# Kernel optimization log

Measured on AMD Instinct MI355X. Metric: run time of the kernel, lower is better.

Reference implementation:

```python
import jax, jax.numpy as jnp
import numpy as np

B, S, D_IN, D_OUT, H = 4, 2048, 1024, 1024, 16
HD = D_OUT // H  # 64


def setup_inputs() -> dict:
    key = jax.random.key(0)
    ks = jax.random.split(key, 6)
    scale_in = 1.0 / np.sqrt(D_IN)
    scale_out = 1.0 / np.sqrt(D_OUT)
    return {
        "x": jax.random.normal(ks[0], (B, S, D_IN), dtype=jnp.float32),
        "Wq": jax.random.normal(ks[1], (D_IN, D_OUT), dtype=jnp.float32) * scale_in,
        "Wk": jax.random.normal(ks[2], (D_IN, D_OUT), dtype=jnp.float32) * scale_in,
        "Wv": jax.random.normal(ks[3], (D_IN, D_OUT), dtype=jnp.float32) * scale_in,
        "Wo": jax.random.normal(ks[4], (D_OUT, D_OUT), dtype=jnp.float32) * scale_out,
        "bo": jax.random.normal(ks[5], (D_OUT,), dtype=jnp.float32) * 0.01,
    }


def reference(x, Wq, Wk, Wv, Wo, bo):
    b, s, _ = x.shape
    # project and split heads: (b, s, d_out) -> (b, h, s, hd)
    def split(t):
        return t.reshape(b, s, H, HD).transpose(0, 2, 1, 3)
    q = split(x @ Wq)
    k = split(x @ Wk)
    v = split(x @ Wv)
    # scaled causal attention scores (b, h, s, s)
    scores = jnp.einsum('bhqd,bhkd->bhqk', q, k) / jnp.sqrt(jnp.float32(HD))
    causal = jnp.tril(jnp.ones((s, s), dtype=bool))
    scores = jnp.where(causal, scores, -jnp.inf)
    weights = jax.nn.softmax(scores, axis=-1)
    # dropout p=0.0 -> identity (eval mode)
    ctx = jnp.einsum('bhqk,bhkd->bhqd', weights, v)
    ctx = ctx.transpose(0, 2, 1, 3).reshape(b, s, D_OUT)
    return ctx @ Wo + bo
```

## Files before the change

### kernel.cpp

```cpp
#include <hip/hip_runtime.h>
#include <stdint.h>

#define DEVINL __device__ __forceinline__

typedef __attribute__((ext_vector_type(8))) __bf16 bf16x8;
typedef __attribute__((ext_vector_type(4))) float f32x4;
typedef __attribute__((ext_vector_type(8))) unsigned short u16x8;
typedef __attribute__((ext_vector_type(2))) unsigned int u32x2;

constexpr int Bc = 4, Sc = 2048, DINc = 1024, Hc = 16;
constexpr float QSCALE = 0.18033688011112042f;

DEVINL unsigned short f2bf(float x) {
  unsigned u = __builtin_bit_cast(unsigned, x);
  u += 0x7fffu + ((u >> 16) & 1u);
  return (unsigned short)(u >> 16);
}

DEVINL unsigned pack_bf16_trunc(float p0, float p1) {
  return __builtin_amdgcn_perm(__builtin_bit_cast(unsigned, p1),
                               __builtin_bit_cast(unsigned, p0), 0x07060302u);
}

DEVINL void gload_lds16(const void* g, void* l) {
  __builtin_amdgcn_global_load_lds(
      (const __attribute__((address_space(1))) void*)g,
      (__attribute__((address_space(3))) void*)l, 16, 0, 0);
}

template <int ROWS>
DEVINL void stage_tile(const unsigned short* g, int ld, void* lds, int tid) {
#pragma unroll
  for (int p = 0; p < ROWS / 32; ++p) {
    int L = (p * 256 + tid) * 16;
    int row = L >> 7;
    int cb = L & 127;
    int scb = cb ^ ((row & 7) << 4);
    gload_lds16((const char*)(g + (size_t)row * ld) + scb, (char*)lds + L);
  }
}

DEVINL bf16x8 read_frag(const void* lds, int row, int kelem) {
  int addr = row * 128 + (((kelem * 2) ^ ((row & 7) << 4)));
  return *(const bf16x8*)((const char*)lds + addr);
}

__global__ __launch_bounds__(256) void prep_inputs(
    const float* __restrict__ x, const float* __restrict__ Wq,
    const float* __restrict__ Wk, const float* __restrict__ Wv,
    const float* __restrict__ Wo, unsigned short* __restrict__ xb,
    unsigned short* __restrict__ wqkvt, unsigned short* __restrict__ wot) {
  __shared__ float t[64][65];
  int bid = blockIdx.x;
  if (bid < 4096) {
    int i = (bid * 256 + threadIdx.x) * 8;
    f32x4 a = *(const f32x4*)(x + i);
    f32x4 b = *(const f32x4*)(x + i + 4);
    u16x8 r;
    r[0] = f2bf(a[0]); r[1] = f2bf(a[1]); r[2] = f2bf(a[2]); r[3] = f2bf(a[3]);
    r[4] = f2bf(b[0]); r[5] = f2bf(b[1]); r[6] = f2bf(b[2]); r[7] = f2bf(b[3]);
    *(u16x8*)(xb + i) = r;
    return;
  }
  int bid2 = bid - 4096;
  int z = bid2 >> 8, rem = bid2 & 255;
  const float* src;
  unsigned short* dst;
  if (z == 0)      { src = Wq; dst = wqkvt; }
  else if (z == 1) { src = Wk; dst = wqkvt + (size_t)1024 * 1024; }
  else if (z == 2) { src = Wv; dst = wqkvt + (size_t)2048 * 1024; }
  else             { src = Wo; dst = wot; }
  int n0 = (rem & 15) * 64, k0 = (rem >> 4) * 64;
  int tx = threadIdx.x & 63, ty = threadIdx.x >> 6;
#pragma unroll
  for (int r = 0; r < 64; r += 4)
    t[r + ty][tx] = src[(size_t)(k0 + r + ty) * 1024 + n0 + tx];
  __syncthreads();
#pragma unroll
  for (int r = 0; r < 64; r += 4)
    dst[(size_t)(n0 + r + ty) * 1024 + k0 + tx] = f2bf(t[tx][r + ty]);
}

__global__ __launch_bounds__(256, 2) void gemm_qkv(
    const unsigned short* __restrict__ A, const unsigned short* __restrict__ Bt,
    unsigned short* __restrict__ qws, unsigned short* __restrict__ kws,
    unsigned short* __restrict__ vtws) {
  __shared__ __align__(16) char lsmem[4 * 128 * 64 * 2];
  unsigned short* lA0 = (unsigned short*)lsmem;
  unsigned short* lB0 = (unsigned short*)(lsmem + 32768);
  int tid = threadIdx.x, lane = tid & 63, wave = tid >> 6;
  int wr = wave >> 1, wc = wave & 1;
  int bm = blockIdx.x, bn = blockIdx.y;
  const unsigned short* Ab = A + (size_t)bm * 128 * 1024;
  const unsigned short* Bb = Bt + (size_t)bn * 128 * 1024;
  int r15 = lane & 15, g4 = lane >> 4, khi = g4 * 8;

  f32x4 acc[4][4];
#pragma unroll
  for (int i = 0; i < 4; ++i)
#pragma unroll
    for (int j = 0; j < 4; ++j) acc[i][j] = (f32x4){0.f, 0.f, 0.f, 0.f};

  int cur = 0;
  stage_tile<128>(Ab, 1024, lA0, tid);
  stage_tile<128>(Bb, 1024, lB0, tid);
#pragma unroll 1
  for (int t = 0; t < 16; ++t) {
    __syncthreads();
    if (t + 1 < 16) {
      stage_tile<128>(Ab + (t + 1) * 64, 1024, lA0 + (cur ^ 1) * 128 * 64, tid);
      stage_tile<128>(Bb + (t + 1) * 64, 1024, lB0 + (cur ^ 1) * 128 * 64, tid);
    }
#pragma unroll
    for (int ks = 0; ks < 2; ++ks) {
      bf16x8 af[4], bfr[4];
#pragma unroll
      for (int i = 0; i < 4; ++i)
        af[i] = read_frag(lA0 + cur * 128 * 64, wr * 64 + i * 16 + r15, ks * 32 + khi);
#pragma unroll
      for (int j = 0; j < 4; ++j)
        bfr[j] = read_frag(lB0 + cur * 128 * 64, wc * 64 + j * 16 + r15, ks * 32 + khi);
      __builtin_amdgcn_s_setprio(1);
#pragma unroll
      for (int i = 0; i < 4; ++i)
#pragma unroll
        for (int j = 0; j < 4; ++j)
          acc[i][j] = __builtin_amdgcn_mfma_f32_16x16x32_bf16(af[i], bfr[j], acc[i][j], 0, 0, 0);
      __builtin_amdgcn_s_setprio(0);
    }
    cur ^= 1;
  }

  int sel = bn >> 3;
  float* sc = (float*)lsmem;
  constexpr int PADW = 132;
  int bq = (bm * 128) >> 11;
#pragma unroll 1
  for (int pass = 0; pass < 2; ++pass) {
    __syncthreads();
    if (wr == pass) {
#pragma unroll
      for (int i = 0; i < 4; ++i)
#pragma unroll
        for (int j = 0; j < 4; ++j)
#pragma unroll
          for (int r = 0; r < 4; ++r) {
            float v = acc[i][j][r];
            if (sel == 0) v *= QSCALE;
            sc[(i * 16 + g4 * 4 + r) * PADW + wc * 64 + j * 16 + r15] = v;
          }
    }
    __syncthreads();
    if (sel < 2) {
      int row = tid >> 2, c0 = (tid & 3) * 32;
      int m = bm * 128 + pass * 64 + row;
      int s = m & 2047;
      int colg = (bn & 7) * 128 + c0;
      int h = colg >> 6, d0 = colg & 63;
      unsigned short* dst =
          (sel == 0 ? qws : kws) + ((size_t)(bq * 16 + h) * 2048 + s) * 64 + d0;
#pragma unroll
      for (int q = 0; q < 4; ++q) {
        f32x4 a = *(const f32x4*)&sc[row * PADW + c0 + q * 8];
        f32x4 b2 = *(const f32x4*)&sc[row * PADW + c0 + q * 8 + 4];
        u16x8 o;
        o[0] = f2bf(a[0]);  o[1] = f2bf(a[1]);  o[2] = f2bf(a[2]);  o[3] = f2bf(a[3]);
        o[4] = f2bf(b2[0]); o[5] = f2bf(b2[1]); o[6] = f2bf(b2[2]); o[7] = f2bf(b2[3]);
        *(u16x8*)(dst + q * 8) = o;
      }
    } else {
      int col = tid >> 1, s0loc = (tid & 1) * 32;
      int colg = (bn & 7) * 128 + col;
      int h = colg >> 6, d = colg & 63;
      int sbase = (bm * 128 + pass * 64 + s0loc) & 2047;
      unsigned short* dst =
          vtws + ((size_t)(bq * 16 + h) * 64 + d) * 2048 + sbase;
#pragma unroll
      for (int q = 0; q < 4; ++q) {
        u16x8 o;
#pragma unroll
        for (int e = 0; e < 8; ++e)
          o[e] = f2bf(sc[(s0loc + q * 8 + e) * PADW + col]);
        *(u16x8*)(dst + q * 8) = o;
      }
    }
  }
}

__global__ __launch_bounds__(256, 3) void attn(
    const unsigned short* __restrict__ qws, const unsigned short* __restrict__ kws,
    const unsigned short* __restrict__ vtws, unsigned short* __restrict__ ctx) {
  __shared__ __align__(16) unsigned short lK[2][64 * 64];
  __shared__ __align__(16) unsigned short lV[2][64 * 64];
  __shared__ __align__(16) unsigned short lP[4][32 * 64];
  int tid = threadIdx.x, lane = tid & 63, wave = tid >> 6;
  int bh = blockIdx.x * 8 + (blockIdx.y & 7);
  int t = 15 - (int)(blockIdx.y >> 3);
  int r15 = lane & 15, g4 = lane >> 4;
  const unsigned short* Kb = kws + (size_t)bh * 2048 * 64;
  const unsigned short* Vb = vtws + (size_t)bh * 64 * 2048;
  int b = bh >> 4, h = bh & 15;
  char* Pw = (char*)&lP[wave][0];

  int q0 = t * 128;
  int myrow0 = q0 + wave * 32;
  const unsigned short* Qb = qws + ((size_t)bh * 2048 + myrow0) * 64;

  bf16x8 qf[2][2];
#pragma unroll
  for (int mf = 0; mf < 2; ++mf)
#pragma unroll
    for (int ks = 0; ks < 2; ++ks)
      qf[mf][ks] = *(const bf16x8*)(Qb + (size_t)(mf * 16 + r15) * 64 + ks * 32 + g4 * 8);

  float m_run[2] = {-1e30f, -1e30f}, l_run[2] = {0.f, 0.f};
  f32x4 o_acc[2][4];
#pragma unroll
  for (int mf = 0; mf < 2; ++mf)
#pragma unroll
    for (int df = 0; df < 4; ++df) o_acc[mf][df] = (f32x4){0.f, 0.f, 0.f, 0.f};

  int nkt = 2 * t + 2;
  int cur = 0;
  stage_tile<64>(Kb, 64, lK[0], tid);
  stage_tile<64>(Vb, 2048, lV[0], tid);

#pragma unroll 1
  for (int kt = 0; kt < nkt; ++kt) {
    __syncthreads();
    if (kt + 1 < nkt) {
      stage_tile<64>(Kb + (size_t)(kt + 1) * 64 * 64, 64, lK[cur ^ 1], tid);
      stage_tile<64>(Vb + (size_t)(kt + 1) * 64, 2048, lV[cur ^ 1], tid);
    }

    f32x4 sacc[2][4];
#pragma unroll
    for (int mf = 0; mf < 2; ++mf)
#pragma unroll
      for (int nf = 0; nf < 4; ++nf) sacc[mf][nf] = (f32x4){0.f, 0.f, 0.f, 0.f};
#pragma unroll
    for (int ks = 0; ks < 2; ++ks) {
      bf16x8 kf[4];
#pragma unroll
      for (int nf = 0; nf < 4; ++nf)
        kf[nf] = read_frag(lK[cur], nf * 16 + r15, ks * 32 + g4 * 8);
      __builtin_amdgcn_s_setprio(1);
#pragma unroll
      for (int mf = 0; mf < 2; ++mf)
#pragma unroll
        for (int nf = 0; nf < 4; ++nf)
          sacc[mf][nf] = __builtin_amdgcn_mfma_f32_16x16x32_bf16(kf[nf], qf[mf][ks], sacc[mf][nf], 0, 0, 0);
      __builtin_amdgcn_s_setprio(0);
    }

    if (kt * 64 + 63 > myrow0) {
#pragma unroll
      for (int mf = 0; mf < 2; ++mf) {
        int q = myrow0 + mf * 16 + r15;
#pragma unroll
        for (int nf = 0; nf < 4; ++nf) {
          int kbase = kt * 64 + nf * 16 + g4 * 4;
#pragma unroll
          for (int r = 0; r < 4; ++r)
            if (kbase + r > q) sacc[mf][nf][r] = -3e38f;
        }
      }
    }

    float tm[2];
#pragma unroll
    for (int mf = 0; mf < 2; ++mf) {
      float a0 = fmaxf(fmaxf(sacc[mf][0][0], sacc[mf][0][1]), fmaxf(sacc[mf][0][2], sacc[mf][0][3]));
      float a1 = fmaxf(fmaxf(sacc[mf][1][0], sacc[mf][1][1]), fmaxf(sacc[mf][1][2], sacc[mf][1][3]));
      float a2 = fmaxf(fmaxf(sacc[mf][2][0], sacc[mf][2][1]), fmaxf(sacc[mf][2][2], sacc[mf][2][3]));
      float a3 = fmaxf(fmaxf(sacc[mf][3][0], sacc[mf][3][1]), fmaxf(sacc[mf][3][2], sacc[mf][3][3]));
      float m = fmaxf(fmaxf(a0, a1), fmaxf(a2, a3));
      m = fmaxf(m, __shfl_xor(m, 16));
      m = fmaxf(m, __shfl_xor(m, 32));
      tm[mf] = m;
    }

    bool ok = (tm[0] <= m_run[0] + 11.5f) & (tm[1] <= m_run[1] + 11.5f);
    if (!__all(ok)) {
#pragma unroll
      for (int mf = 0; mf < 2; ++mf) {
        float mn = fmaxf(m_run[mf], tm[mf]);
        float a = __builtin_amdgcn_exp2f(m_run[mf] - mn);
        m_run[mf] = mn;
        l_run[mf] *= a;
        float av[4];
#pragma unroll
        for (int r = 0; r < 4; ++r)
          av[r] = __shfl(a, (g4 * 4 + r) | (lane & 48));
#pragma unroll
        for (int df = 0; df < 4; ++df)
#pragma unroll
          for (int r = 0; r < 4; ++r) o_acc[mf][df][r] *= av[r];
      }
    }

    float rs[2] = {0.f, 0.f};
#pragma unroll
    for (int mf = 0; mf < 2; ++mf) {
      int prow = mf * 16 + r15;
      char* Prow = Pw + prow * 128;
      int sw = (prow & 7) << 4;
#pragma unroll
      for (int nf = 0; nf < 4; ++nf) {
        float p0 = __builtin_amdgcn_exp2f(sacc[mf][nf][0] - m_run[mf]);
        float p1 = __builtin_amdgcn_exp2f(sacc[mf][nf][1] - m_run[mf]);
        float p2 = __builtin_amdgcn_exp2f(sacc[mf][nf][2] - m_run[mf]);
        float p3 = __builtin_amdgcn_exp2f(sacc[mf][nf][3] - m_run[mf]);
        rs[mf] += (p0 + p1) + (p2 + p3);
        *(u32x2*)(Prow + (((nf * 16 + g4 * 4) * 2) ^ sw)) =
            (u32x2){pack_bf16_trunc(p0, p1), pack_bf16_trunc(p2, p3)};
      }
      float s = rs[mf];
      s += __shfl_xor(s, 16);
      s += __shfl_xor(s, 32);
      l_run[mf] += s;
    }

#pragma unroll
    for (int ks = 0; ks < 2; ++ks) {
      bf16x8 vf[4];
#pragma unroll
      for (int df = 0; df < 4; ++df)
        vf[df] = read_frag(lV[cur], df * 16 + r15, ks * 32 + g4 * 8);
      bf16x8 pf[2];
#pragma unroll
      for (int mf = 0; mf < 2; ++mf)
        pf[mf] = read_frag(Pw, mf * 16 + r15, ks * 32 + g4 * 8);
      __builtin_amdgcn_s_setprio(1);
#pragma unroll
      for (int mf = 0; mf < 2; ++mf)
#pragma unroll
        for (int df = 0; df < 4; ++df)
          o_acc[mf][df] = __builtin_amdgcn_mfma_f32_16x16x32_bf16(pf[mf], vf[df], o_acc[mf][df], 0, 0, 0);
      __builtin_amdgcn_s_setprio(0);
    }
    cur ^= 1;
  }

#pragma unroll
  for (int mf = 0; mf < 2; ++mf) {
    float rl = 1.f / l_run[mf];
    float rv[4];
#pragma unroll
    for (int r = 0; r < 4; ++r)
      rv[r] = __shfl(rl, (g4 * 4 + r) | (lane & 48));
#pragma unroll
    for (int r = 0; r < 4; ++r) {
      int row = myrow0 + mf * 16 + g4 * 4 + r;
#pragma unroll
      for (int df = 0; df < 4; ++df)
        ctx[((size_t)(b * 2048 + row)) * 1024 + h * 64 + df * 16 + r15] =
            f2bf(o_acc[mf][df][r] * rv[r]);
    }
  }
}

__global__ __launch_bounds__(256, 2) void gemm_out(
    const unsigned short* __restrict__ A, const unsigned short* __restrict__ Bt,
    const float* __restrict__ bo, float* __restrict__ out) {
  __shared__ __align__(16) unsigned short lA[2][128 * 64];
  __shared__ __align__(16) unsigned short lB[2][128 * 64];
  int tid = threadIdx.x, lane = tid & 63, wave = tid >> 6;
  int wr = wave >> 1, wc = wave & 1;
  int bm = blockIdx.x, bn = blockIdx.y;
  const unsigned short* Ab = A + (size_t)bm * 128 * 1024;
  const unsigned short* Bb = Bt + (size_t)bn * 128 * 1024;
  int r15 = lane & 15, khi = (lane >> 4) * 8;

  f32x4 acc[4][4];
#pragma unroll
  for (int i = 0; i < 4; ++i)
#pragma unroll
    for (int j = 0; j < 4; ++j) acc[i][j] = (f32x4){0.f, 0.f, 0.f, 0.f};

  int cur = 0;
  stage_tile<128>(Ab, 1024, lA[0], tid);
  stage_tile<128>(Bb, 1024, lB[0], tid);
#pragma unroll 1
  for (int t = 0; t < 16; ++t) {
    __syncthreads();
    if (t + 1 < 16) {
      stage_tile<128>(Ab + (t + 1) * 64, 1024, lA[cur ^ 1], tid);
      stage_tile<128>(Bb + (t + 1) * 64, 1024, lB[cur ^ 1], tid);
    }
#pragma unroll
    for (int ks = 0; ks < 2; ++ks) {
      bf16x8 af[4], bfr[4];
#pragma unroll
      for (int i = 0; i < 4; ++i)
        af[i] = read_frag(lA[cur], wr * 64 + i * 16 + r15, ks * 32 + khi);
#pragma unroll
      for (int j = 0; j < 4; ++j)
        bfr[j] = read_frag(lB[cur], wc * 64 + j * 16 + r15, ks * 32 + khi);
      __builtin_amdgcn_s_setprio(1);
#pragma unroll
      for (int i = 0; i < 4; ++i)
#pragma unroll
        for (int j = 0; j < 4; ++j)
          acc[i][j] = __builtin_amdgcn_mfma_f32_16x16x32_bf16(af[i], bfr[j], acc[i][j], 0, 0, 0);
      __builtin_amdgcn_s_setprio(0);
    }
    cur ^= 1;
  }

  int nbase = bn * 128 + wc * 64;
  int mbase = bm * 128 + wr * 64;
#pragma unroll
  for (int j = 0; j < 4; ++j) {
    int n = nbase + j * 16 + r15;
    float bias = bo[n];
#pragma unroll
    for (int i = 0; i < 4; ++i)
#pragma unroll
      for (int r = 0; r < 4; ++r) {
        int m = mbase + i * 16 + (lane >> 4) * 4 + r;
        out[(size_t)m * 1024 + n] = acc[i][j][r] + bias;
      }
  }
}

extern "C" void kernel_launch(void* const* d_in, const int* in_sizes, int n_in,
                              void* d_out, int out_size, void* d_ws, size_t ws_size,
                              hipStream_t stream) {
  const float* x = (const float*)d_in[0];
  const float* Wq = (const float*)d_in[1];
  const float* Wk = (const float*)d_in[2];
  const float* Wv = (const float*)d_in[3];
  const float* Wo = (const float*)d_in[4];
  const float* bo = (const float*)d_in[5];
  float* out = (float*)d_out;

  char* ws = (char*)d_ws;
  unsigned short* xb    = (unsigned short*)(ws);
  unsigned short* wqkvt = (unsigned short*)(ws + (16u << 20));
  unsigned short* wot   = (unsigned short*)(ws + (22u << 20));
  unsigned short* qws   = (unsigned short*)(ws + (24u << 20));
  unsigned short* kws   = (unsigned short*)(ws + (40u << 20));
  unsigned short* vtws  = (unsigned short*)(ws + (56u << 20));
  unsigned short* ctxws = (unsigned short*)(ws + (72u << 20));

  prep_inputs<<<dim3(5120), dim3(256), 0, stream>>>(x, Wq, Wk, Wv, Wo, xb, wqkvt, wot);

  gemm_qkv<<<dim3(64, 24), dim3(256), 0, stream>>>(xb, wqkvt, qws, kws, vtws);
  attn<<<dim3(8, 128), dim3(256), 0, stream>>>(qws, kws, vtws, ctxws);
  gemm_out<<<dim3(64, 8), dim3(256), 0, stream>>>(ctxws, wot, bo, out);
}
```

Before: 166.1 us.

## Single-buffer LDS in projection GEMMs to fit three blocks per CU

Replaces the double-buffered LDS staging in the QKV and output-projection GEMMs with a single buffer. Each k-step now loads, syncs, computes, then syncs again, and launch bounds rise from 2 to 3 blocks per CU. The goal is more resident blocks hiding memory latency through occupancy instead of software prefetch. The cost is that load/compute overlap inside a block is lost, a second barrier is added per iteration, and register pressure under the tighter launch bound may cause spills.

```diff
diff --git a/kernel.cpp b/kernel.cpp
--- a/kernel.cpp
+++ b/kernel.cpp
@@ -81,13 +81,13 @@
     dst[(size_t)(n0 + r + ty) * 1024 + k0 + tx] = f2bf(t[tx][r + ty]);
 }
 
-__global__ __launch_bounds__(256, 2) void gemm_qkv(
+__global__ __launch_bounds__(256, 3) void gemm_qkv(
     const unsigned short* __restrict__ A, const unsigned short* __restrict__ Bt,
     unsigned short* __restrict__ qws, unsigned short* __restrict__ kws,
     unsigned short* __restrict__ vtws) {
-  __shared__ __align__(16) char lsmem[4 * 128 * 64 * 2];
+  __shared__ __align__(16) char lsmem[33792];
   unsigned short* lA0 = (unsigned short*)lsmem;
-  unsigned short* lB0 = (unsigned short*)(lsmem + 32768);
+  unsigned short* lB0 = (unsigned short*)(lsmem + 16384);
   int tid = threadIdx.x, lane = tid & 63, wave = tid >> 6;
   int wr = wave >> 1, wc = wave & 1;
   int bm = blockIdx.x, bn = blockIdx.y;
@@ -101,25 +101,20 @@
 #pragma unroll
     for (int j = 0; j < 4; ++j) acc[i][j] = (f32x4){0.f, 0.f, 0.f, 0.f};
 
-  int cur = 0;
-  stage_tile<128>(Ab, 1024, lA0, tid);
-  stage_tile<128>(Bb, 1024, lB0, tid);
 #pragma unroll 1
   for (int t = 0; t < 16; ++t) {
-    __syncthreads();
-    if (t + 1 < 16) {
-      stage_tile<128>(Ab + (t + 1) * 64, 1024, lA0 + (cur ^ 1) * 128 * 64, tid);
-      stage_tile<128>(Bb + (t + 1) * 64, 1024, lB0 + (cur ^ 1) * 128 * 64, tid);
-    }
+    stage_tile<128>(Ab + t * 64, 1024, lA0, tid);
+    stage_tile<128>(Bb + t * 64, 1024, lB0, tid);
+    __syncthreads();
 #pragma unroll
     for (int ks = 0; ks < 2; ++ks) {
       bf16x8 af[4], bfr[4];
 #pragma unroll
       for (int i = 0; i < 4; ++i)
-        af[i] = read_frag(lA0 + cur * 128 * 64, wr * 64 + i * 16 + r15, ks * 32 + khi);
+        af[i] = read_frag(lA0, wr * 64 + i * 16 + r15, ks * 32 + khi);
 #pragma unroll
       for (int j = 0; j < 4; ++j)
-        bfr[j] = read_frag(lB0 + cur * 128 * 64, wc * 64 + j * 16 + r15, ks * 32 + khi);
+        bfr[j] = read_frag(lB0, wc * 64 + j * 16 + r15, ks * 32 + khi);
       __builtin_amdgcn_s_setprio(1);
 #pragma unroll
       for (int i = 0; i < 4; ++i)
@@ -128,7 +123,7 @@
           acc[i][j] = __builtin_amdgcn_mfma_f32_16x16x32_bf16(af[i], bfr[j], acc[i][j], 0, 0, 0);
       __builtin_amdgcn_s_setprio(0);
     }
-    cur ^= 1;
+    __syncthreads();
   }
 
   int sel = bn >> 3;
@@ -360,11 +355,11 @@
   }
 }
 
-__global__ __launch_bounds__(256, 2) void gemm_out(
+__global__ __launch_bounds__(256, 3) void gemm_out(
     const unsigned short* __restrict__ A, const unsigned short* __restrict__ Bt,
     const float* __restrict__ bo, float* __restrict__ out) {
-  __shared__ __align__(16) unsigned short lA[2][128 * 64];
-  __shared__ __align__(16) unsigned short lB[2][128 * 64];
+  __shared__ __align__(16) unsigned short lA[128 * 64];
+  __shared__ __align__(16) unsigned short lB[128 * 64];
   int tid = threadIdx.x, lane = tid & 63, wave = tid >> 6;
   int wr = wave >> 1, wc = wave & 1;
   int bm = blockIdx.x, bn = blockIdx.y;
@@ -378,25 +373,20 @@
 #pragma unroll
     for (int j = 0; j < 4; ++j) acc[i][j] = (f32x4){0.f, 0.f, 0.f, 0.f};
 
-  int cur = 0;
-  stage_tile<128>(Ab, 1024, lA[0], tid);
-  stage_tile<128>(Bb, 1024, lB[0], tid);
 #pragma unroll 1
   for (int t = 0; t < 16; ++t) {
-    __syncthreads();
-    if (t + 1 < 16) {
-      stage_tile<128>(Ab + (t + 1) * 64, 1024, lA[cur ^ 1], tid);
-      stage_tile<128>(Bb + (t + 1) * 64, 1024, lB[cur ^ 1], tid);
-    }
+    stage_tile<128>(Ab + t * 64, 1024, lA, tid);
+    stage_tile<128>(Bb + t * 64, 1024, lB, tid);
+    __syncthreads();
 #pragma unroll
     for (int ks = 0; ks < 2; ++ks) {
       bf16x8 af[4], bfr[4];
 #pragma unroll
       for (int i = 0; i < 4; ++i)
-        af[i] = read_frag(lA[cur], wr * 64 + i * 16 + r15, ks * 32 + khi);
+        af[i] = read_frag(lA, wr * 64 + i * 16 + r15, ks * 32 + khi);
 #pragma unroll
       for (int j = 0; j < 4; ++j)
-        bfr[j] = read_frag(lB[cur], wc * 64 + j * 16 + r15, ks * 32 + khi);
+        bfr[j] = read_frag(lB, wc * 64 + j * 16 + r15, ks * 32 + khi);
       __builtin_amdgcn_s_setprio(1);
 #pragma unroll
       for (int i = 0; i < 4; ++i)
@@ -405,7 +395,7 @@
           acc[i][j] = __builtin_amdgcn_mfma_f32_16x16x32_bf16(af[i], bfr[j], acc[i][j], 0, 0, 0);
       __builtin_amdgcn_s_setprio(0);
     }
-    cur ^= 1;
+    __syncthreads();
   }
 
   int nbase = bn * 128 + wc * 64;
```

Result: no change. 165.1 us, median of 2 (-0.6%).
